# Kernel tuning notes

Hardware: AMD Instinct MI355X
Metric: run time of the kernel (lower is better)

## Reference

```python
import jax, jax.numpy as jnp
import numpy as np


def setup_inputs() -> dict:
    key = jax.random.key(0)
    k1, k2, k3, k4 = jax.random.split(key, 4)
    B, S, H, P = 8, 2048, 1024, 4096
    hidden_states = jax.random.normal(k1, (B, S, H), dtype=jnp.float32)
    pairs = jax.random.randint(k2, (B, P, 2), 0, S, dtype=jnp.int64)
    # classifier params: Linear(2H -> H), Linear(H -> 2). Stored as (in, out).
    W1 = jax.random.normal(k3, (2 * H, H), dtype=jnp.float32) * (1.0 / np.sqrt(2 * H))
    b1 = jnp.zeros((H,), dtype=jnp.float32)
    W2 = jax.random.normal(k4, (H, 2), dtype=jnp.float32) * (1.0 / np.sqrt(H))
    b2 = jnp.zeros((2,), dtype=jnp.float32)
    return {"hidden_states": hidden_states, "pairs": pairs,
            "W1": W1, "b1": b1, "W2": W2, "b2": b2}


def reference(hidden_states, pairs, W1, b1, W2, b2):
    # Gather pair embeddings: (B, P, H) each.
    emb1 = jnp.take_along_axis(hidden_states, pairs[:, :, 0:1], axis=1)
    emb2 = jnp.take_along_axis(hidden_states, pairs[:, :, 1:2], axis=1)
    pair_emb = jnp.concatenate([emb1, emb2], axis=-1)  # (B, P, 2H)
    h = jnp.einsum('bpi,ih->bph', pair_emb, W1) + b1
    h = jax.nn.gelu(h, approximate=False)  # torch nn.GELU default is exact erf
    # Dropout is identity at inference.
    logits = jnp.einsum('bph,ho->bpo', h, W2) + b2  # (B, P, 2)
    return logits
```

## Files before the change

### kernel.cpp

```cpp
#include <hip/hip_runtime.h>
#include <hip/hip_bf16.h>

#define B_  8
#define S_  2048
#define H_  1024
#define P_  4096
#define K_  2048
#define M_  32768

typedef unsigned short u16;
using bf16x8 = __attribute__((ext_vector_type(8))) short;
using f32x4  = __attribute__((ext_vector_type(4))) float;

#define AS1 __attribute__((address_space(1)))
#define AS3 __attribute__((address_space(3)))

__device__ inline u16 f2bf(float f) {
  union { float f; unsigned u; } c; c.f = f;
  unsigned u = c.u;
  unsigned r = (u + 0x7fffu + ((u >> 16) & 1u)) >> 16;
  return (u16)r;
}

__global__ void cvt_hidden_k(const float4* __restrict__ src,
                             ushort4* __restrict__ dst, int n4) {
  int i = blockIdx.x * blockDim.x + threadIdx.x;
  int stride = gridDim.x * blockDim.x;
  for (; i < n4; i += stride) {
    float4 v = src[i];
    ushort4 o;
    o.x = f2bf(v.x); o.y = f2bf(v.y); o.z = f2bf(v.z); o.w = f2bf(v.w);
    dst[i] = o;
  }
}

__global__ void transp_w1_k(const float* __restrict__ w1, u16* __restrict__ w1t) {
  __shared__ float tile[32][33];
  int n0 = blockIdx.x * 32;
  int k0 = blockIdx.y * 32;
  int tx = threadIdx.x;
  int ty = threadIdx.y;
#pragma unroll
  for (int i = 0; i < 32; i += 8)
    tile[ty + i][tx] = w1[(size_t)(k0 + ty + i) * H_ + n0 + tx];
  __syncthreads();
#pragma unroll
  for (int i = 0; i < 32; i += 8)
    w1t[(size_t)(n0 + ty + i) * K_ + k0 + tx] = f2bf(tile[tx][ty + i]);
}

__global__ __launch_bounds__(512, 2) void gemm_k(
    const u16*  __restrict__ hidB,
    const u16*  __restrict__ w1t,
    const int*  __restrict__ pairs,
    const float* __restrict__ b1,
    const float2* __restrict__ w2,
    float*      __restrict__ part)
{
  __shared__ u16 lds[65536];

#define REG(SLOT, KS, AB) ((((SLOT)*2 + (KS))*2 + (AB)) * 8192)

  int orig = blockIdx.x;
  int bid = (orig & 7) * 64 + (orig >> 3);
  int nt = bid & 3;
  int mt = bid >> 2;
  int n0 = nt * 256;
  int m0 = mt * 256;
  int bI = m0 >> 12;
  int pp = m0 & 4095;

  int t = threadIdx.x;
  int w = t >> 6;
  int l = t & 63;
  int lr = l & 15;
  int lj = l >> 4;
  int wr = w >> 2;
  int wn = w & 3;

  int slot8 = (lj ^ ((l >> 1) & 3)) * 8;
  int gsrc = (l & 3) ^ ((l >> 3) & 3);

  int r0 = w * 16 + (l >> 2);
  int r1 = 128 + r0;

  int2 sv0 = ((const int2*)pairs)[bI * P_ + pp + r0];
  int2 sv1 = ((const int2*)pairs)[bI * P_ + pp + r1];

  const u16* hidBase = hidB + ((size_t)bI << 21);

  f32x4 acc[8][4];
#pragma unroll
  for (int i = 0; i < 8; ++i)
#pragma unroll
    for (int j = 0; j < 4; ++j)
      acc[i][j] = (f32x4){0.f, 0.f, 0.f, 0.f};

  auto STAGE_A = [&](int base, int tile, int ks) {
    int k = tile * 64 + ks * 32;
    int kcol = k & 1023;
    int half = k >> 10;
    int sA0 = half ? sv0.y : sv0.x;
    int sA1 = half ? sv1.y : sv1.x;
    int dst = base + w * 512 + l * 8;
    __builtin_amdgcn_global_load_lds(
        (const AS1 void*)(hidBase + (((size_t)sA0) << 10) + kcol + gsrc * 8),
        (AS3 void*)&lds[dst], 16, 0, 0);
    __builtin_amdgcn_global_load_lds(
        (const AS1 void*)(hidBase + (((size_t)sA1) << 10) + kcol + gsrc * 8),
        (AS3 void*)&lds[dst + 4096], 16, 0, 0);
  };
  auto STAGE_B = [&](int base, int tile, int ks) {
    int k = tile * 64 + ks * 32;
    int dst = base + w * 512 + l * 8;
    __builtin_amdgcn_global_load_lds(
        (const AS1 void*)(w1t + (size_t)(n0 + r0) * K_ + k + gsrc * 8),
        (AS3 void*)&lds[dst], 16, 0, 0);
    __builtin_amdgcn_global_load_lds(
        (const AS1 void*)(w1t + (size_t)(n0 + r1) * K_ + k + gsrc * 8),
        (AS3 void*)&lds[dst + 4096], 16, 0, 0);
  };

#define VM8 asm volatile("s_waitcnt vmcnt(8)" ::: "memory")
#define VM4 asm volatile("s_waitcnt vmcnt(4)" ::: "memory")
#define VM0 asm volatile("s_waitcnt vmcnt(0)" ::: "memory")

#define PHASE(SLOT, KS, STAGEOP, WAITOP)                                       \
  {                                                                            \
    bf16x8 af[2][4], bv[4];                                                    \
    _Pragma("unroll")                                                          \
    for (int MH = 0; MH < 2; ++MH)                                             \
      _Pragma("unroll")                                                        \
      for (int mi = 0; mi < 4; ++mi)                                           \
        af[MH][mi] = *(const bf16x8*)&lds[REG(SLOT, KS, 0) +                   \
            (wr * 128 + MH * 64 + mi * 16 + lr) * 32 + slot8];                 \
    _Pragma("unroll")                                                          \
    for (int ni = 0; ni < 4; ++ni)                                             \
      bv[ni] = *(const bf16x8*)&lds[REG(SLOT, KS, 1) +                         \
          (wn * 64 + ni * 16 + lr) * 32 + slot8];                              \
    STAGEOP;                                                                   \
    WAITOP;                                                                    \
    __builtin_amdgcn_s_barrier();                                              \
    asm volatile("s_waitcnt lgkmcnt(0)" ::: "memory");                         \
    __builtin_amdgcn_sched_barrier(0);                                         \
    __builtin_amdgcn_s_setprio(1);                                             \
    _Pragma("unroll")                                                          \
    for (int MH = 0; MH < 2; ++MH)                                             \
      _Pragma("unroll")                                                        \
      for (int mi = 0; mi < 4; ++mi)                                           \
        _Pragma("unroll")                                                      \
        for (int ni = 0; ni < 4; ++ni)                                         \
          acc[MH * 4 + mi][ni] = __builtin_amdgcn_mfma_f32_16x16x32_bf16(      \
              af[MH][mi], bv[ni], acc[MH * 4 + mi][ni], 0, 0, 0);              \
    __builtin_amdgcn_s_setprio(0);                                             \
    __builtin_amdgcn_s_barrier();                                              \
  }

  STAGE_A(REG(0, 0, 0), 0, 0); STAGE_B(REG(0, 0, 1), 0, 0);
  STAGE_A(REG(0, 1, 0), 0, 1); STAGE_B(REG(0, 1, 1), 0, 1);
  STAGE_A(REG(1, 0, 0), 1, 0); STAGE_B(REG(1, 0, 1), 1, 0);
  VM8;
  __builtin_amdgcn_s_barrier();

  for (int u = 0; u < 15; ++u) {
    int t1 = 2 * u + 1, t2 = 2 * u + 2, t3 = 2 * u + 3;
    PHASE(0, 0, { STAGE_A(REG(1,1,0), t1, 1); STAGE_B(REG(1,1,1), t1, 1); }, VM8);
    PHASE(0, 1, { STAGE_A(REG(0,0,0), t2, 0); STAGE_B(REG(0,0,1), t2, 0); }, VM8);
    PHASE(1, 0, { STAGE_A(REG(0,1,0), t2, 1); STAGE_B(REG(0,1,1), t2, 1); }, VM8);
    PHASE(1, 1, { STAGE_A(REG(1,0,0), t3, 0); STAGE_B(REG(1,0,1), t3, 0); }, VM8);
  }
  PHASE(0, 0, { STAGE_A(REG(1,1,0), 31, 1); STAGE_B(REG(1,1,1), 31, 1); }, VM8);
  PHASE(0, 1, , VM8);
  PHASE(1, 0, , VM4);
  PHASE(1, 1, , VM0);
#undef PHASE

  int q = nt * 4 + wn;
  float2* pOut = (float2*)part;
#pragma unroll
  for (int mi = 0; mi < 8; ++mi) {
    float s0[4] = {0.f, 0.f, 0.f, 0.f};
    float s1[4] = {0.f, 0.f, 0.f, 0.f};
#pragma unroll
    for (int ni = 0; ni < 4; ++ni) {
      int n = n0 + wn * 64 + ni * 16 + lr;
      float bb = b1[n];
      float2 wv = w2[n];
#pragma unroll
      for (int j = 0; j < 4; ++j) {
        float x = acc[mi][ni][j] + bb;
        float g = 0.5f * x * (1.0f + erff(x * 0.70710678118654752f));
        s0[j] += g * wv.x;
        s1[j] += g * wv.y;
      }
    }
#pragma unroll
    for (int off = 1; off < 16; off <<= 1) {
#pragma unroll
      for (int j = 0; j < 4; ++j) {
        s0[j] += __shfl_xor(s0[j], off, 64);
        s1[j] += __shfl_xor(s1[j], off, 64);
      }
    }
    if (lr == 0) {
#pragma unroll
      for (int j = 0; j < 4; ++j) {
        int m = m0 + wr * 128 + mi * 16 + lj * 4 + j;
        pOut[((size_t)q << 15) + m] = make_float2(s0[j], s1[j]);
      }
    }
  }
}

__global__ void reduce_k(const float2* __restrict__ part,
                         const float* __restrict__ b2,
                         float2* __restrict__ out) {
  int m = blockIdx.x * blockDim.x + threadIdx.x;
  if (m >= M_) return;
  float a0 = b2[0], a1 = b2[1];
#pragma unroll
  for (int q = 0; q < 16; ++q) {
    float2 v = part[((size_t)q << 15) + m];
    a0 += v.x; a1 += v.y;
  }
  out[m] = make_float2(a0, a1);
}

extern "C" void kernel_launch(void* const* d_in, const int* in_sizes, int n_in,
                              void* d_out, int out_size, void* d_ws, size_t ws_size,
                              hipStream_t stream) {
  const float* hidden = (const float*)d_in[0];
  const int*   pairs  = (const int*)d_in[1];
  const float* W1     = (const float*)d_in[2];
  const float* b1     = (const float*)d_in[3];
  const float* W2     = (const float*)d_in[4];
  const float* b2     = (const float*)d_in[5];
  float* out = (float*)d_out;

  u16* hidB = (u16*)d_ws;
  u16* w1t  = hidB + (size_t)B_ * S_ * H_;
  float* part = (float*)(w1t + (size_t)H_ * K_);

  int n4 = (B_ * S_ * H_) / 4;
  cvt_hidden_k<<<4096, 256, 0, stream>>>((const float4*)hidden, (ushort4*)hidB, n4);
  transp_w1_k<<<dim3(H_ / 32, K_ / 32), dim3(32, 8), 0, stream>>>(W1, w1t);
  gemm_k<<<(M_ / 256) * (H_ / 256), 512, 0, stream>>>(
      hidB, w1t, pairs, b1, (const float2*)W2, part);
  reduce_k<<<(M_ + 255) / 256, 256, 0, stream>>>(
      (const float2*)part, b2, (float2*)out);
}
```

Before: 174.4 us.

## Restructure GEMM pipeline into triple-buffered K=32 tiles with split A/B staging

```diff
diff --git a/kernel.cpp b/kernel.cpp
--- a/kernel.cpp
+++ b/kernel.cpp
@@ -7,6 +7,7 @@
 #define P_  4096
 #define K_  2048
 #define M_  32768
+#define NT_ 64
 
 typedef unsigned short u16;
 using bf16x8 = __attribute__((ext_vector_type(8))) short;
@@ -57,9 +58,9 @@
     const float2* __restrict__ w2,
     float*      __restrict__ part)
 {
-  __shared__ u16 lds[65536];
-
-#define REG(SLOT, KS, AB) ((((SLOT)*2 + (KS))*2 + (AB)) * 8192)
+  __shared__ u16 lds[3 * 16384];
+
+#define RNG(TB) ((unsigned)((TB) % 3) * 16384u)
 
   int orig = blockIdx.x;
   int bid = (orig & 7) * 64 + (orig >> 3);
@@ -96,13 +97,14 @@
     for (int j = 0; j < 4; ++j)
       acc[i][j] = (f32x4){0.f, 0.f, 0.f, 0.f};
 
-  auto STAGE_A = [&](int base, int tile, int ks) {
-    int k = tile * 64 + ks * 32;
-    int kcol = k & 1023;
-    int half = k >> 10;
+  auto STAGE_Aop = [&](int TB) {
+    unsigned base = RNG(TB);
+    int k0 = TB * 32;
+    int kcol = k0 & 1023;
+    int half = k0 >> 10;
     int sA0 = half ? sv0.y : sv0.x;
     int sA1 = half ? sv1.y : sv1.x;
-    int dst = base + w * 512 + l * 8;
+    unsigned dst = base + (unsigned)(w * 512 + l * 8);
     __builtin_amdgcn_global_load_lds(
         (const AS1 void*)(hidBase + (((size_t)sA0) << 10) + kcol + gsrc * 8),
         (AS3 void*)&lds[dst], 16, 0, 0);
@@ -110,70 +112,77 @@
         (const AS1 void*)(hidBase + (((size_t)sA1) << 10) + kcol + gsrc * 8),
         (AS3 void*)&lds[dst + 4096], 16, 0, 0);
   };
-  auto STAGE_B = [&](int base, int tile, int ks) {
-    int k = tile * 64 + ks * 32;
-    int dst = base + w * 512 + l * 8;
-    __builtin_amdgcn_global_load_lds(
-        (const AS1 void*)(w1t + (size_t)(n0 + r0) * K_ + k + gsrc * 8),
+  auto STAGE_Bop = [&](int TB) {
+    unsigned base = RNG(TB) + 8192u;
+    int k0 = TB * 32;
+    unsigned dst = base + (unsigned)(w * 512 + l * 8);
+    __builtin_amdgcn_global_load_lds(
+        (const AS1 void*)(w1t + (size_t)(n0 + r0) * K_ + k0 + gsrc * 8),
         (AS3 void*)&lds[dst], 16, 0, 0);
     __builtin_amdgcn_global_load_lds(
-        (const AS1 void*)(w1t + (size_t)(n0 + r1) * K_ + k + gsrc * 8),
+        (const AS1 void*)(w1t + (size_t)(n0 + r1) * K_ + k0 + gsrc * 8),
         (AS3 void*)&lds[dst + 4096], 16, 0, 0);
   };
 
-#define VM8 asm volatile("s_waitcnt vmcnt(8)" ::: "memory")
 #define VM4 asm volatile("s_waitcnt vmcnt(4)" ::: "memory")
 #define VM0 asm volatile("s_waitcnt vmcnt(0)" ::: "memory")
 
-#define PHASE(SLOT, KS, STAGEOP, WAITOP)                                       \
+#define TILEBODY(T, STA, STB, WAITOP)                                          \
   {                                                                            \
-    bf16x8 af[2][4], bv[4];                                                    \
-    _Pragma("unroll")                                                          \
-    for (int MH = 0; MH < 2; ++MH)                                             \
+    unsigned rg_ = RNG(T);                                                     \
+    bf16x8 bv[4], af[4];                                                       \
+          \
+    _Pragma("unroll")                                                          \
+    for (int mi = 0; mi < 4; ++mi)                                             \
+      af[mi] = *(const bf16x8*)&lds[rg_ +                                      \
+          (unsigned)(wr * 128 + mi * 16 + lr) * 32u + slot8];                  \
+    _Pragma("unroll")                                                          \
+    for (int ni = 0; ni < 4; ++ni)                                             \
+      bv[ni] = *(const bf16x8*)&lds[rg_ + 8192u +                              \
+          (unsigned)(wn * 64 + ni * 16 + lr) * 32u + slot8];                   \
+    STA;                                                                       \
+    __builtin_amdgcn_s_barrier();                                              \
+    __builtin_amdgcn_s_setprio(1);                                             \
+    _Pragma("unroll")                                                          \
+    for (int mi = 0; mi < 4; ++mi)                                             \
       _Pragma("unroll")                                                        \
-      for (int mi = 0; mi < 4; ++mi)                                           \
-        af[MH][mi] = *(const bf16x8*)&lds[REG(SLOT, KS, 0) +                   \
-            (wr * 128 + MH * 64 + mi * 16 + lr) * 32 + slot8];                 \
-    _Pragma("unroll")                                                          \
-    for (int ni = 0; ni < 4; ++ni)                                             \
-      bv[ni] = *(const bf16x8*)&lds[REG(SLOT, KS, 1) +                         \
-          (wn * 64 + ni * 16 + lr) * 32 + slot8];                              \
-    STAGEOP;                                                                   \
+      for (int ni = 0; ni < 4; ++ni)                                           \
+        acc[mi][ni] = __builtin_amdgcn_mfma_f32_16x16x32_bf16(                 \
+            af[mi], bv[ni], acc[mi][ni], 0, 0, 0);                             \
+    __builtin_amdgcn_s_setprio(0);                                             \
+    __builtin_amdgcn_s_barrier();                                              \
+         \
+    _Pragma("unroll")                                                          \
+    for (int mi = 0; mi < 4; ++mi)                                             \
+      af[mi] = *(const bf16x8*)&lds[rg_ +                                      \
+          (unsigned)(wr * 128 + 64 + mi * 16 + lr) * 32u + slot8];             \
+    STB;                                                                       \
     WAITOP;                                                                    \
     __builtin_amdgcn_s_barrier();                                              \
-    asm volatile("s_waitcnt lgkmcnt(0)" ::: "memory");                         \
-    __builtin_amdgcn_sched_barrier(0);                                         \
     __builtin_amdgcn_s_setprio(1);                                             \
     _Pragma("unroll")                                                          \
-    for (int MH = 0; MH < 2; ++MH)                                             \
+    for (int mi = 0; mi < 4; ++mi)                                             \
       _Pragma("unroll")                                                        \
-      for (int mi = 0; mi < 4; ++mi)                                           \
-        _Pragma("unroll")                                                      \
-        for (int ni = 0; ni < 4; ++ni)                                         \
-          acc[MH * 4 + mi][ni] = __builtin_amdgcn_mfma_f32_16x16x32_bf16(      \
-              af[MH][mi], bv[ni], acc[MH * 4 + mi][ni], 0, 0, 0);              \
+      for (int ni = 0; ni < 4; ++ni)                                           \
+        acc[4 + mi][ni] = __builtin_amdgcn_mfma_f32_16x16x32_bf16(             \
+            af[mi], bv[ni], acc[4 + mi][ni], 0, 0, 0);                         \
     __builtin_amdgcn_s_setprio(0);                                             \
     __builtin_amdgcn_s_barrier();                                              \
   }
 
-  STAGE_A(REG(0, 0, 0), 0, 0); STAGE_B(REG(0, 0, 1), 0, 0);
-  STAGE_A(REG(0, 1, 0), 0, 1); STAGE_B(REG(0, 1, 1), 0, 1);
-  STAGE_A(REG(1, 0, 0), 1, 0); STAGE_B(REG(1, 0, 1), 1, 0);
-  VM8;
+  STAGE_Aop(0); STAGE_Bop(0);
+  STAGE_Aop(1); STAGE_Bop(1);
+  VM4;
   __builtin_amdgcn_s_barrier();
 
-  for (int u = 0; u < 15; ++u) {
-    int t1 = 2 * u + 1, t2 = 2 * u + 2, t3 = 2 * u + 3;
-    PHASE(0, 0, { STAGE_A(REG(1,1,0), t1, 1); STAGE_B(REG(1,1,1), t1, 1); }, VM8);
-    PHASE(0, 1, { STAGE_A(REG(0,0,0), t2, 0); STAGE_B(REG(0,0,1), t2, 0); }, VM8);
-    PHASE(1, 0, { STAGE_A(REG(0,1,0), t2, 1); STAGE_B(REG(0,1,1), t2, 1); }, VM8);
-    PHASE(1, 1, { STAGE_A(REG(1,0,0), t3, 0); STAGE_B(REG(1,0,1), t3, 0); }, VM8);
-  }
-  PHASE(0, 0, { STAGE_A(REG(1,1,0), 31, 1); STAGE_B(REG(1,1,1), 31, 1); }, VM8);
-  PHASE(0, 1, , VM8);
-  PHASE(1, 0, , VM4);
-  PHASE(1, 1, , VM0);
-#undef PHASE
+  for (int u = 0; u < 31; ++u) {
+    int t0 = 2 * u, t1 = 2 * u + 1;
+    TILEBODY(t0, STAGE_Aop(t0 + 2), STAGE_Bop(t0 + 2), VM4);
+    TILEBODY(t1, STAGE_Aop(t1 + 2), STAGE_Bop(t1 + 2), VM4);
+  }
+  TILEBODY(62, , , VM0);
+  TILEBODY(63, , , );
+#undef TILEBODY
 
   int q = nt * 4 + wn;
   float2* pOut = (float2*)part;
```

Result: slower. 178.4 us (+2.3%).
